# Kernel tuning notes

Hardware: AMD Instinct MI355X
Metric: run time of the kernel (lower is better)

## Reference

```python
import jax, jax.numpy as jnp
import numpy as np

HID = 256
STYLE_DIM = 64
NUM_STYLES = 8
IN_DIM = 3 + STYLE_DIM


def setup_inputs() -> dict:
    key = jax.random.key(0)
    ks = jax.random.split(key, 12)
    B, H, W = 2, 512, 512
    rgb = jax.random.uniform(ks[0], (B, 3, H, W), dtype=jnp.float32)
    style_idx = jax.random.randint(ks[1], (B,), 0, NUM_STYLES, dtype=jnp.int32)
    # style embedding table (torch init: normal std=0.01)
    emb_table = 0.01 * jax.random.normal(ks[2], (NUM_STYLES, STYLE_DIM), dtype=jnp.float32)
    # kaiming-normal (fan_in, relu gain sqrt(2)) weights stored as [in, out]
    def kaiming(k, fan_in, fan_out):
        std = np.sqrt(2.0 / fan_in)
        return std * jax.random.normal(k, (fan_in, fan_out), dtype=jnp.float32)
    W0 = kaiming(ks[3], IN_DIM, HID); b0 = jnp.zeros((HID,), jnp.float32)
    W1 = kaiming(ks[4], HID, HID);    b1 = jnp.zeros((HID,), jnp.float32)
    W2 = kaiming(ks[5], HID, HID);    b2 = jnp.zeros((HID,), jnp.float32)
    W3 = kaiming(ks[6], HID, 3);      b3 = jnp.zeros((3,), jnp.float32)
    return {"rgb": rgb, "style_idx": style_idx, "emb_table": emb_table,
            "W0": W0, "b0": b0, "W1": W1, "b1": b1,
            "W2": W2, "b2": b2, "W3": W3, "b3": b3}


def reference(rgb, style_idx, emb_table, W0, b0, W1, b1, W2, b2, W3, b3):
    B, C, H, W_ = rgb.shape  # CHW image input
    # [B,3,H,W] -> [B*H*W, 3]
    rgb_flat = jnp.transpose(rgb, (0, 2, 3, 1)).reshape(-1, 3)
    # style embedding lookup, broadcast per pixel
    emb = emb_table[style_idx]                              # [B, style_dim]
    emb = jnp.broadcast_to(emb[:, None, :], (B, H * W_, STYLE_DIM)).reshape(-1, STYLE_DIM)
    x = jnp.concatenate([rgb_flat, emb], axis=-1)           # [N, 67]
    gelu = lambda t: jax.nn.gelu(t, approximate=False)      # torch nn.GELU default (erf)
    x = gelu(x @ W0 + b0)
    x = gelu(x @ W1 + b1)
    x = gelu(x @ W2 + b2)
    out_flat = jax.nn.sigmoid(x @ W3 + b3)                  # [N, 3]
    out = out_flat.reshape(B, H, W_, 3).transpose(0, 3, 1, 2)
    return out
```

## Files before the change

### kernel.cpp

```cpp
#include <hip/hip_runtime.h>

#define HW  (512*512)

typedef _Float16 half8  __attribute__((__vector_size__(16)));
typedef float    floatx4 __attribute__((__vector_size__(16)));

__device__ __forceinline__ float gelu_f(float x){
    float x2 = x * x;
    float q  = __builtin_fmaf(x2, -0.1029432f, -2.3022079f);
    float e  = __builtin_amdgcn_exp2f(x * q);
    return x * __builtin_amdgcn_rcpf(1.0f + e);
}

__device__ __forceinline__ float sigmoid_f(float x){
    float e = __builtin_amdgcn_exp2f(-1.44269504f * x);
    return __builtin_amdgcn_rcpf(1.0f + e);
}

__device__ __forceinline__ int swz(int row){
    return ((row >> 2) & 3) << 4;
}

__global__ void prep_all(const float* __restrict__ W1, const float* __restrict__ W2,
                         const float* __restrict__ W3, const float* __restrict__ emb,
                         const int* __restrict__ sidx, const float* __restrict__ W0,
                         const float* __restrict__ b0,
                         _Float16* __restrict__ wp, float* __restrict__ c0){
    __shared__ float ld[32][68];
    int blk = blockIdx.x;
    int tid = threadIdx.x;
    if (blk < 64){
        int mat = blk >> 5;
        int g   = blk & 31;
        int ks  = g >> 2;
        int ntq = g & 3;
        const float* W = mat ? W2 : W1;
        int row = tid >> 3;
        int c8  = (tid & 7) * 8;
        const float* src = &W[(ks*32 + row)*256 + ntq*64 + c8];
        *(floatx4*)&ld[row][c8]     = *(const floatx4*)src;
        *(floatx4*)&ld[row][c8 + 4] = *(const floatx4*)(src + 4);
        __syncthreads();
        int lane = tid & 63;
        int nt_l = tid >> 6;
        half8 h;
        #pragma unroll
        for (int j = 0; j < 8; j++)
            h[j] = (_Float16)ld[(lane >> 4)*8 + j][nt_l*16 + (lane & 15)];
        _Float16* dst = wp + mat*65536 + (ks*16 + ntq*4 + nt_l)*512 + lane*8;
        *(half8*)dst = h;
    } else if (blk < 80){
        int i    = (blk - 64)*256 + tid;
        int j    = i & 7;
        int lane = (i >> 3) & 63;
        int ks   = i >> 9;
        int k = ks*32 + ((lane >> 4) << 3) + j;
        int n = lane & 15;
        wp[131072 + i] = (_Float16)((n < 3) ? W3[k*3 + n] : 0.0f);
    } else {
        int b = blk - 80;
        int s = sidx[b];
        float acc = b0[tid];
        #pragma unroll 8
        for (int d = 0; d < 64; d++)
            acc = fmaf(emb[s*64 + d], W0[(3 + d)*256 + tid], acc);
        c0[b*256 + tid] = acc;
    }
}

__global__ __launch_bounds__(256, 4)
void nilut_main(const float* __restrict__ rgb,
                const float* __restrict__ W0,
                const float* __restrict__ b1v,
                const float* __restrict__ b2v,
                const float* __restrict__ b3v,
                const _Float16* __restrict__ wp,
                const float* __restrict__ c0,
                float* __restrict__ out){
    __shared__ __align__(16) _Float16 act[64 * 256];
    __shared__ __align__(16) float    w0s[1024];
    __shared__ __align__(16) float    rgbs[192];

    const int tid = threadIdx.x;
    const int wg  = blockIdx.x;
    const int pixbase = wg * 64;
    const int b   = pixbase >> 18;
    const int hw0 = pixbase & (HW - 1);

    #pragma unroll
    for (int r = 0; r < 4; r++){
        int q = r*256 + tid;
        w0s[q] = (q < 768) ? W0[q] : c0[b*256 + (q - 768)];
    }
    if (tid < 192){
        int c = tid >> 6, row = tid & 63;
        rgbs[tid] = rgb[b*3*HW + c*HW + hw0 + row];
    }
    __syncthreads();

    {
        int ng = tid & 31;
        int rg = tid >> 5;
        floatx4 cw[4][2];
        #pragma unroll
        for (int p = 0; p < 4; p++){
            cw[p][0] = *(const floatx4*)&w0s[p*256 + ng*8];
            cw[p][1] = *(const floatx4*)&w0s[p*256 + ng*8 + 4];
        }
        #pragma unroll
        for (int hf = 0; hf < 2; hf++){
            floatx4 rv[3];
            #pragma unroll
            for (int c = 0; c < 3; c++)
                rv[c] = *(const floatx4*)&rgbs[c*64 + rg*8 + hf*4];
            #pragma unroll
            for (int r4 = 0; r4 < 4; r4++){
                int row = rg*8 + hf*4 + r4;
                float rr = rv[0][r4], gg = rv[1][r4], bb = rv[2][r4];
                half8 v;
                #pragma unroll
                for (int j = 0; j < 8; j++){
                    int hi = j >> 2, lo = j & 3;
                    float z = fmaf(rr, cw[0][hi][lo],
                              fmaf(gg, cw[1][hi][lo],
                              fmaf(bb, cw[2][hi][lo], cw[3][hi][lo])));
                    v[j] = (_Float16)gelu_f(z);
                }
                *(half8*)&act[row*256 + ((ng*8) ^ swz(row))] = v;
            }
        }
    }
    __syncthreads();

    const int lane = tid & 63;
    const int wv   = tid >> 6;
    const int ln15 = lane & 15;
    const int quad = lane >> 4;
    const int q8   = quad * 8;
    const int qr   = quad * 4;
    const int sA   = swz(ln15);

    const _Float16* wl  = wp;
    const float* bias   = b1v;
    const int cb16  = wv * 4;

    int ebase[4];
    #pragma unroll
    for (int nt = 0; nt < 4; nt++)
        ebase[nt] = qr*256 + (((cb16 + nt)*16 + ln15) ^ (quad << 4));

    #pragma unroll 1
    for (int L = 0; L < 2; L++){
        floatx4 acc[4][4];
        #pragma unroll
        for (int nt = 0; nt < 4; nt++){
            float bv = bias[(cb16 + nt)*16 + ln15];
            #pragma unroll
            for (int m = 0; m < 4; m++)
                acc[m][nt] = (floatx4){bv, bv, bv, bv};
        }

        const half8* wp8 = (const half8*)wl;
        #pragma unroll 2
        for (int ks = 0; ks < 8; ks++){
            int k0 = (ks*32 + q8) ^ sA;
            half8 a[4];
            #pragma unroll
            for (int m = 0; m < 4; m++)
                a[m] = *(const half8*)&act[(m*16 + ln15)*256 + k0];
            #pragma unroll
            for (int nt = 0; nt < 4; nt++){
                half8 bf = wp8[(ks*16 + cb16 + nt)*64 + lane];
                #pragma unroll
                for (int m = 0; m < 4; m++)
                    acc[m][nt] = __builtin_amdgcn_mfma_f32_16x16x32_f16(a[m], bf, acc[m][nt], 0, 0, 0);
            }
        }
        __syncthreads();
        #pragma unroll
        for (int nt = 0; nt < 4; nt++){
            #pragma unroll
            for (int m = 0; m < 4; m++){
                #pragma unroll
                for (int r = 0; r < 4; r++)
                    act[ebase[nt] + m*4096 + r*256] = (_Float16)gelu_f(acc[m][nt][r]);
            }
        }
        __syncthreads();
        wl = wp + 65536;
        bias = b2v;
    }

    {
        const half8* wp8 = (const half8*)(wp + 131072);
        int rbf = wv * 16;
        floatx4 ac = (floatx4){0.f,0.f,0.f,0.f};
        #pragma unroll
        for (int ks = 0; ks < 8; ks++){
            int k0 = (ks*32 + q8) ^ sA;
            half8 a  = *(const half8*)&act[(rbf + ln15)*256 + k0];
            half8 bf = wp8[ks*64 + lane];
            ac = __builtin_amdgcn_mfma_f32_16x16x32_f16(a, bf, ac, 0, 0, 0);
        }
        if (ln15 < 3){
            float bv = b3v[ln15];
            #pragma unroll
            for (int r = 0; r < 4; r++){
                int row0 = rbf + qr + r;
                w0s[ln15*64 + row0] = sigmoid_f(ac[r] + bv);
            }
        }
        __syncthreads();
        if (tid < 48){
            int c  = tid >> 4;
            int i2 = tid & 15;
            float4* dst = (float4*)(out + (b*3 + c)*HW + hw0);
            dst[i2] = ((float4*)(w0s + c*64))[i2];
        }
    }
}

extern "C" void kernel_launch(void* const* d_in, const int* in_sizes, int n_in,
                              void* d_out, int out_size, void* d_ws, size_t ws_size,
                              hipStream_t stream){
    const float* rgb = (const float*)d_in[0];
    const int*  sidx = (const int*) d_in[1];
    const float* emb = (const float*)d_in[2];
    const float* W0  = (const float*)d_in[3];
    const float* b0  = (const float*)d_in[4];
    const float* W1  = (const float*)d_in[5];
    const float* b1  = (const float*)d_in[6];
    const float* W2  = (const float*)d_in[7];
    const float* b2  = (const float*)d_in[8];
    const float* W3  = (const float*)d_in[9];
    const float* b3  = (const float*)d_in[10];
    float* out = (float*)d_out;

    _Float16* wp = (_Float16*)d_ws;
    float*    c0 = (float*)((char*)d_ws + 270336);

    int n_pix = in_sizes[0] / 3;
    prep_all<<<82, 256, 0, stream>>>(W1, W2, W3, emb, sidx, W0, b0, wp, c0);
    nilut_main<<<n_pix / 64, 256, 0, stream>>>(rgb, W0, b1, b2, b3, wp, c0, out);
}
```

Before: 272.7 us.

## Swap MFMA operand roles so outputs are pixel-contiguous with new XOR swizzle

Computes each hidden layer transposed: weights become the A operand and activations the B operand, so each lane's accumulator holds four consecutive output channels for one pixel. Epilogue GELU results are packed with cvt_pkrtz and written as 8-byte vector stores instead of scalar half stores. The LDS activation swizzle changes to an XOR on 16-byte chunks by row&7, with matching read offsets. This aims to cut LDS store instructions and bank conflicts in the epilogue, at the cost of round-toward-zero conversion instead of round-to-nearest.

```diff
diff --git a/kernel.cpp b/kernel.cpp
--- a/kernel.cpp
+++ b/kernel.cpp
@@ -3,6 +3,8 @@
 #define HW  (512*512)
 
 typedef _Float16 half8  __attribute__((__vector_size__(16)));
+typedef _Float16 half4  __attribute__((__vector_size__(8)));
+typedef _Float16 half2_t __attribute__((__vector_size__(4)));
 typedef float    floatx4 __attribute__((__vector_size__(16)));
 
 __device__ __forceinline__ float gelu_f(float x){
@@ -17,9 +19,6 @@
     return __builtin_amdgcn_rcpf(1.0f + e);
 }
 
-__device__ __forceinline__ int swz(int row){
-    return ((row >> 2) & 3) << 4;
-}
 
 __global__ void prep_all(const float* __restrict__ W1, const float* __restrict__ W2,
                          const float* __restrict__ W3, const float* __restrict__ emb,
@@ -126,7 +125,7 @@
                               fmaf(bb, cw[2][hi][lo], cw[3][hi][lo])));
                     v[j] = (_Float16)gelu_f(z);
                 }
-                *(half8*)&act[row*256 + ((ng*8) ^ swz(row))] = v;
+                *(half8*)&act[row*256 + ((ng ^ (row & 7)) << 3)] = v;
             }
         }
     }
@@ -136,54 +135,63 @@
     const int wv   = tid >> 6;
     const int ln15 = lane & 15;
     const int quad = lane >> 4;
-    const int q8   = quad * 8;
     const int qr   = quad * 4;
-    const int sA   = swz(ln15);
+    const int sx   = ln15 & 7;
+    const int qx8  = (quad ^ (sx & 3)) * 8;
+    const int kb32 = ((sx >> 2) & 1) << 5;
+
+    int pbq[4];
+    #pragma unroll
+    for (int pt = 0; pt < 4; pt++)
+        pbq[pt] = (pt*16 + ln15)*256 + qx8;
+
+    const int qh = quad >> 1, qs = (quad & 1) * 4;
+    int eb[4];
+    #pragma unroll
+    for (int pt = 0; pt < 4; pt++)
+        eb[pt] = (pt*16 + ln15)*256 + qs;
 
     const _Float16* wl  = wp;
     const float* bias   = b1v;
-    const int cb16  = wv * 4;
-
-    int ebase[4];
-    #pragma unroll
-    for (int nt = 0; nt < 4; nt++)
-        ebase[nt] = qr*256 + (((cb16 + nt)*16 + ln15) ^ (quad << 4));
-
     #pragma unroll 1
     for (int L = 0; L < 2; L++){
         floatx4 acc[4][4];
         #pragma unroll
-        for (int nt = 0; nt < 4; nt++){
-            float bv = bias[(cb16 + nt)*16 + ln15];
-            #pragma unroll
-            for (int m = 0; m < 4; m++)
-                acc[m][nt] = (floatx4){bv, bv, bv, bv};
+        for (int mtl = 0; mtl < 4; mtl++){
+            floatx4 bv = *(const floatx4*)&bias[(wv*4 + mtl)*16 + qr];
+            #pragma unroll
+            for (int pt = 0; pt < 4; pt++)
+                acc[pt][mtl] = bv;
         }
 
         const half8* wp8 = (const half8*)wl;
         #pragma unroll 2
         for (int ks = 0; ks < 8; ks++){
-            int k0 = (ks*32 + q8) ^ sA;
-            half8 a[4];
-            #pragma unroll
-            for (int m = 0; m < 4; m++)
-                a[m] = *(const half8*)&act[(m*16 + ln15)*256 + k0];
-            #pragma unroll
-            for (int nt = 0; nt < 4; nt++){
-                half8 bf = wp8[(ks*16 + cb16 + nt)*64 + lane];
+            int t = (ks << 5) ^ kb32;
+            half8 bfr[4];
+            #pragma unroll
+            for (int pt = 0; pt < 4; pt++)
+                bfr[pt] = *(const half8*)&act[pbq[pt] + t];
+            #pragma unroll
+            for (int mtl = 0; mtl < 4; mtl++){
+                half8 af = wp8[(ks*16 + wv*4 + mtl)*64 + lane];
                 #pragma unroll
-                for (int m = 0; m < 4; m++)
-                    acc[m][nt] = __builtin_amdgcn_mfma_f32_16x16x32_f16(a[m], bf, acc[m][nt], 0, 0, 0);
+                for (int pt = 0; pt < 4; pt++)
+                    acc[pt][mtl] = __builtin_amdgcn_mfma_f32_16x16x32_f16(af, bfr[pt], acc[pt][mtl], 0, 0, 0);
             }
         }
         __syncthreads();
         #pragma unroll
-        for (int nt = 0; nt < 4; nt++){
-            #pragma unroll
-            for (int m = 0; m < 4; m++){
-                #pragma unroll
-                for (int r = 0; r < 4; r++)
-                    act[ebase[nt] + m*4096 + r*256] = (_Float16)gelu_f(acc[m][nt][r]);
+        for (int mtl = 0; mtl < 4; mtl++){
+            int cx = (((wv*4 + mtl)*2 + qh) ^ sx) << 3;
+            #pragma unroll
+            for (int pt = 0; pt < 4; pt++){
+                floatx4 v = acc[pt][mtl];
+                half2_t g01 = __builtin_amdgcn_cvt_pkrtz(gelu_f(v[0]), gelu_f(v[1]));
+                half2_t g23 = __builtin_amdgcn_cvt_pkrtz(gelu_f(v[2]), gelu_f(v[3]));
+                half4 h;
+                h[0] = g01[0]; h[1] = g01[1]; h[2] = g23[0]; h[3] = g23[1];
+                *(half4*)&act[eb[pt] + cx] = h;
             }
         }
         __syncthreads();
@@ -193,22 +201,18 @@
 
     {
         const half8* wp8 = (const half8*)(wp + 131072);
-        int rbf = wv * 16;
         floatx4 ac = (floatx4){0.f,0.f,0.f,0.f};
+        int pb = (wv*16 + ln15)*256 + qx8;
         #pragma unroll
         for (int ks = 0; ks < 8; ks++){
-            int k0 = (ks*32 + q8) ^ sA;
-            half8 a  = *(const half8*)&act[(rbf + ln15)*256 + k0];
-            half8 bf = wp8[ks*64 + lane];
-            ac = __builtin_amdgcn_mfma_f32_16x16x32_f16(a, bf, ac, 0, 0, 0);
-        }
-        if (ln15 < 3){
-            float bv = b3v[ln15];
-            #pragma unroll
-            for (int r = 0; r < 4; r++){
-                int row0 = rbf + qr + r;
-                w0s[ln15*64 + row0] = sigmoid_f(ac[r] + bv);
-            }
+            half8 bfr = *(const half8*)&act[pb + ((ks << 5) ^ kb32)];
+            half8 af  = wp8[ks*64 + lane];
+            ac = __builtin_amdgcn_mfma_f32_16x16x32_f16(af, bfr, ac, 0, 0, 0);
+        }
+        if (quad == 0){
+            #pragma unroll
+            for (int r = 0; r < 3; r++)
+                w0s[r*64 + wv*16 + ln15] = sigmoid_f(ac[r] + b3v[r]);
         }
         __syncthreads();
         if (tid < 48){
```

Result: faster. 266.2 us (-2.4%).
